# Kernel tuning notes

Hardware: AMD Instinct MI355X
Metric: run time of the kernel (lower is better)

## Reference

```python
import jax, jax.numpy as jnp
import numpy as np

B, C_IN, C_OUT, H, W = 8, 64, 64, 128, 128
G, K, PAD = 8, 3, 1
CG_OUT = C_OUT // G   # 8
CG_IN = C_IN // G     # 8


def setup_inputs() -> dict:
    key = jax.random.key(0)
    ks = jax.random.split(key, 6)
    x = jax.random.normal(ks[0], (B, C_IN, H, W), dtype=jnp.float32)
    # grouped 1x1 conv weights, stored as (groups, out_per_group, in_per_group)
    scale = (2.0 / C_OUT) ** 0.5  # kaiming fan_out
    Wq = jax.random.normal(ks[1], (G, CG_OUT, CG_IN), dtype=jnp.float32) * scale
    Wk = jax.random.normal(ks[2], (G, CG_OUT, CG_IN), dtype=jnp.float32) * scale
    Wv = jax.random.normal(ks[3], (G, CG_OUT, CG_IN), dtype=jnp.float32) * scale
    h_emb = jax.random.normal(ks[4], (G, CG_OUT // 2, 1, 1, K, 1), dtype=jnp.float32)
    w_emb = jax.random.normal(ks[5], (G, CG_OUT // 2, 1, 1, 1, K), dtype=jnp.float32)
    return {"x": x, "Wq": Wq, "Wk": Wk, "Wv": Wv, "h_emb": h_emb, "w_emb": w_emb}


def _gconv1x1(x, Wt):
    # grouped 1x1 conv: x (B,C,H,W) -> (B,G,Cg,H,W)
    b, c, h, w = x.shape
    xg = x.reshape(b, G, c // G, h, w)
    return jnp.einsum('bgihw,goi->bgohw', xg, Wt)


def _unfold(t):
    # t: (B,G,Cg,H+2p,W+2p) -> (B,G,Cg,H,W,K*K), window index = i*K + j (h-major,
    # matching torch unfold(2).unfold(3).view)
    slices = [t[..., i:i + H, j:j + W] for i in range(K) for j in range(K)]
    return jnp.stack(slices, axis=-1)


def reference(x, Wq, Wk, Wv, h_emb, w_emb):
    x_pad = jnp.pad(x, ((0, 0), (0, 0), (PAD, PAD), (PAD, PAD)))
    q = _gconv1x1(x, Wq)            # (B,G,Cg,H,W)
    kf = _gconv1x1(x_pad, Wk)       # (B,G,Cg,H+2,W+2)
    vf = _gconv1x1(x_pad, Wv)
    kp = _unfold(kf)                # (B,G,Cg,H,W,K^2)
    vp = _unfold(vf)
    # relative position embedding: h half broadcast over w, w half over h
    he = jnp.broadcast_to(h_emb, (G, CG_OUT // 2, 1, 1, K, K))
    we = jnp.broadcast_to(w_emb, (G, CG_OUT // 2, 1, 1, K, K))
    emb = jnp.concatenate([he, we], axis=1).reshape(G, CG_OUT, 1, 1, K * K)
    logits = q[..., None] * (kp + emb[None])       # (B,G,Cg,H,W,K^2)
    attn = jax.nn.softmax(logits, axis=-1)
    out = jnp.sum(attn * vp, axis=-1)              # (B,G,Cg,H,W)
    return out.reshape(x.shape[0], C_OUT, H, W)
```

## Files before the change

### kernel.cpp

```cpp
#include <hip/hip_runtime.h>


typedef float v2f __attribute__((ext_vector_type(2)));
typedef float v4f __attribute__((ext_vector_type(4)));

#define HH 128
#define WW 128
#define HW (HH * WW)
#define PT 34
#define PTS 38
#define LOG2E 1.44269504088896f

__device__ __forceinline__ float sload(float v) {
    return __uint_as_float(__builtin_amdgcn_readfirstlane(__float_as_uint(v)));
}

__device__ __forceinline__ v4f exp2v4(v4f a) {
    v4f r;
    r.x = __builtin_amdgcn_exp2f(a.x);
    r.y = __builtin_amdgcn_exp2f(a.y);
    r.z = __builtin_amdgcn_exp2f(a.z);
    r.w = __builtin_amdgcn_exp2f(a.w);
    return r;
}

__global__ __launch_bounds__(256) void sab_fused(
    const float* __restrict__ x,
    const float* __restrict__ Wq,
    const float* __restrict__ Wk,
    const float* __restrict__ Wv,
    const float* __restrict__ h_emb,
    const float* __restrict__ w_emb,
    float* __restrict__ out)
{
    __shared__ v2f kv[2][PT][PTS];

    const int bid0 = blockIdx.x;
    const int work = (bid0 & 7) * 512 + (bid0 >> 3);
    const int c0   = (work & 3) << 1;
    const int tile = (work >> 2) & 15;
    const int bg   = work >> 6;
    const int g    = bg & 7;
    const int h0   = (tile >> 2) << 5;
    const int w0   = (tile & 3) << 5;
    const int tid  = threadIdx.x;
    const int ty   = tid >> 3;
    const int x0   = (tid & 7) << 2;

    float wk[2][8], wv[2][8], wq[2][8], eb[2][9];
    #pragma unroll
    for (int cc = 0; cc < 2; cc++) {
        const int c = c0 + cc;
        #pragma unroll
        for (int i = 0; i < 8; i++) {
            wk[cc][i] = sload(Wk[g * 64 + c * 8 + i]);
            wv[cc][i] = sload(Wv[g * 64 + c * 8 + i]);
            wq[cc][i] = sload(Wq[g * 64 + c * 8 + i]);
        }
        #pragma unroll
        for (int p = 0; p < 9; p++) {
            eb[cc][p] = sload((c < 4) ? h_emb[(g * 4 + c) * 3 + p / 3]
                                      : w_emb[(g * 4 + c - 4) * 3 + p % 3]);
        }
    }

    const float* xb = x + (size_t)bg * 8 * HW;
    const int ibase = (h0 + ty) * WW + (w0 + x0);

    v4f xi[8];
    #pragma unroll
    for (int i = 0; i < 8; i++)
        xi[i] = *reinterpret_cast<const v4f*>(xb + i * HW + ibase);

    v4f kk0 = 0.f, vv0 = 0.f, qq0 = 0.f, kk1 = 0.f, vv1 = 0.f, qq1 = 0.f;
    #pragma unroll
    for (int i = 0; i < 8; i++) {
        const v4f xv = xi[i];
        kk0 += wk[0][i] * xv;  vv0 += wv[0][i] * xv;  qq0 += wq[0][i] * xv;
        kk1 += wk[1][i] * xv;  vv1 += wv[1][i] * xv;  qq1 += wq[1][i] * xv;
    }
    #pragma unroll
    for (int px = 0; px < 4; px++) {
        kv[0][ty + 1][x0 + 1 + px] = (v2f){kk0[px], vv0[px]};
        kv[1][ty + 1][x0 + 1 + px] = (v2f){kk1[px], vv1[px]};
    }
    const v4f q0 = qq0 * LOG2E;
    const v4f q1 = qq1 * LOG2E;

    if (tid < 132) {
        int hpy, hpx;
        if (tid < 34)       { hpy = 0;        hpx = tid; }
        else if (tid < 68)  { hpy = 33;       hpx = tid - 34; }
        else if (tid < 100) { hpy = tid - 67; hpx = 0; }
        else                { hpy = tid - 99; hpx = 33; }
        const int gh = h0 + hpy - 1, gw = w0 + hpx - 1;
        const bool ok = (gh >= 0) & (gh < HH) & (gw >= 0) & (gw < WW);
        const int base = gh * WW + gw;
        float hk0 = 0.f, hv0 = 0.f, hk1 = 0.f, hv1 = 0.f;
        #pragma unroll
        for (int i = 0; i < 8; i++) {
            const float xv = ok ? xb[i * HW + base] : 0.0f;
            hk0 = fmaf(wk[0][i], xv, hk0);
            hv0 = fmaf(wv[0][i], xv, hv0);
            hk1 = fmaf(wk[1][i], xv, hk1);
            hv1 = fmaf(wv[1][i], xv, hv1);
        }
        kv[0][hpy][hpx] = (v2f){hk0, hv0};
        kv[1][hpy][hpx] = (v2f){hk1, hv1};
    }
    __syncthreads();

    v4f s0 = 0.f, o0 = 0.f, s1 = 0.f, o1 = 0.f;
    #pragma unroll
    for (int dh = 0; dh < 3; dh++) {
        #pragma unroll
        for (int cc = 0; cc < 2; cc++) {
            const v2f* row = &kv[cc][ty + dh][x0];
            const v4f a = *reinterpret_cast<const v4f*>(row);
            const v4f bq = *reinterpret_cast<const v4f*>(row + 2);
            const v4f cq = *reinterpret_cast<const v4f*>(row + 4);

            const v4f kd0 = {a.x, a.z, bq.x, bq.z};
            const v4f vd0 = {a.y, a.w, bq.y, bq.w};
            const v4f kd1 = {a.z, bq.x, bq.z, cq.x};
            const v4f vd1 = {a.w, bq.y, bq.w, cq.y};
            const v4f kd2 = {bq.x, bq.z, cq.x, cq.z};
            const v4f vd2 = {bq.y, bq.w, cq.y, cq.w};

            const v4f q4 = cc ? q1 : q0;
            v4f e;
            e = exp2v4(q4 * (kd0 + eb[cc][dh * 3 + 0]));
            if (cc) { s1 += e; o1 += e * vd0; } else { s0 += e; o0 += e * vd0; }
            e = exp2v4(q4 * (kd1 + eb[cc][dh * 3 + 1]));
            if (cc) { s1 += e; o1 += e * vd1; } else { s0 += e; o0 += e * vd1; }
            e = exp2v4(q4 * (kd2 + eb[cc][dh * 3 + 2]));
            if (cc) { s1 += e; o1 += e * vd2; } else { s0 += e; o0 += e * vd2; }
        }
    }

    v4f r0, r1;
    #pragma unroll
    for (int px = 0; px < 4; px++) {
        r0[px] = o0[px] * __builtin_amdgcn_rcpf(s0[px]);
        r1[px] = o1[px] * __builtin_amdgcn_rcpf(s1[px]);
    }
    *reinterpret_cast<v4f*>(out + (size_t)(bg * 8 + c0 + 0) * HW + ibase) = r0;
    *reinterpret_cast<v4f*>(out + (size_t)(bg * 8 + c0 + 1) * HW + ibase) = r1;
}

extern "C" void kernel_launch(void* const* d_in, const int* in_sizes, int n_in,
                              void* d_out, int out_size, void* d_ws, size_t ws_size,
                              hipStream_t stream) {
    const float* x    = (const float*)d_in[0];
    const float* Wq   = (const float*)d_in[1];
    const float* Wk   = (const float*)d_in[2];
    const float* Wv   = (const float*)d_in[3];
    const float* h_e  = (const float*)d_in[4];
    const float* w_e  = (const float*)d_in[5];
    float* out = (float*)d_out;

    dim3 grid(8 * 8 * 16 * 4);
    dim3 block(256);
    sab_fused<<<grid, block, 0, stream>>>(x, Wq, Wk, Wv, h_e, w_e, out);
}
```

Measured before the change: 28.75 us.

## Loop over all output-channel pairs per block to reuse loaded input tile

Each block now handles all four channel pairs of a group for its spatial tile, looping over chunks instead of launching a separate block per pair. The 8-channel input tile and halo values are loaded once into registers and reused across the four chunks, which cuts redundant global reads of x by four. The trade-offs are a grid four times smaller (1024 blocks), extra barriers between chunks that serialise the shared-memory reuse, and more live registers.

```diff
diff --git a/kernel.cpp b/kernel.cpp
--- a/kernel.cpp
+++ b/kernel.cpp
@@ -36,10 +36,9 @@
     __shared__ v2f kv[2][PT][PTS];
 
     const int bid0 = blockIdx.x;
-    const int work = (bid0 & 7) * 512 + (bid0 >> 3);
-    const int c0   = (work & 3) << 1;
-    const int tile = (work >> 2) & 15;
-    const int bg   = work >> 6;
+    const int work = (bid0 & 7) * 128 + (bid0 >> 3);
+    const int tile = work & 15;
+    const int bg   = work >> 4;
     const int g    = bg & 7;
     const int h0   = (tile >> 2) << 5;
     const int w0   = (tile & 3) << 5;
@@ -47,105 +46,119 @@
     const int ty   = tid >> 3;
     const int x0   = (tid & 7) << 2;
 
-    float wk[2][8], wv[2][8], wq[2][8], eb[2][9];
-    #pragma unroll
-    for (int cc = 0; cc < 2; cc++) {
-        const int c = c0 + cc;
-        #pragma unroll
-        for (int i = 0; i < 8; i++) {
-            wk[cc][i] = sload(Wk[g * 64 + c * 8 + i]);
-            wv[cc][i] = sload(Wv[g * 64 + c * 8 + i]);
-            wq[cc][i] = sload(Wq[g * 64 + c * 8 + i]);
-        }
-        #pragma unroll
-        for (int p = 0; p < 9; p++) {
-            eb[cc][p] = sload((c < 4) ? h_emb[(g * 4 + c) * 3 + p / 3]
-                                      : w_emb[(g * 4 + c - 4) * 3 + p % 3]);
-        }
-    }
-
     const float* xb = x + (size_t)bg * 8 * HW;
     const int ibase = (h0 + ty) * WW + (w0 + x0);
+
+    int hpy = 0, hpx = 0;
+    const bool is_halo = tid < 132;
+    if (is_halo) {
+        if (tid < 34)       { hpy = 0;        hpx = tid; }
+        else if (tid < 68)  { hpy = 33;       hpx = tid - 34; }
+        else if (tid < 100) { hpy = tid - 67; hpx = 0; }
+        else                { hpy = tid - 99; hpx = 33; }
+    }
+    const int hgh = h0 + hpy - 1, hgw = w0 + hpx - 1;
+    const bool hok = is_halo & (hgh >= 0) & (hgh < HH) & (hgw >= 0) & (hgw < WW);
+    const int hbase = hgh * WW + hgw;
+
+    float hx[8];
+    #pragma unroll
+    for (int i = 0; i < 8; i++)
+        hx[i] = hok ? xb[i * HW + hbase] : 0.0f;
 
     v4f xi[8];
     #pragma unroll
     for (int i = 0; i < 8; i++)
         xi[i] = *reinterpret_cast<const v4f*>(xb + i * HW + ibase);
 
-    v4f kk0 = 0.f, vv0 = 0.f, qq0 = 0.f, kk1 = 0.f, vv1 = 0.f, qq1 = 0.f;
-    #pragma unroll
-    for (int i = 0; i < 8; i++) {
-        const v4f xv = xi[i];
-        kk0 += wk[0][i] * xv;  vv0 += wv[0][i] * xv;  qq0 += wq[0][i] * xv;
-        kk1 += wk[1][i] * xv;  vv1 += wv[1][i] * xv;  qq1 += wq[1][i] * xv;
-    }
-    #pragma unroll
-    for (int px = 0; px < 4; px++) {
-        kv[0][ty + 1][x0 + 1 + px] = (v2f){kk0[px], vv0[px]};
-        kv[1][ty + 1][x0 + 1 + px] = (v2f){kk1[px], vv1[px]};
-    }
-    const v4f q0 = qq0 * LOG2E;
-    const v4f q1 = qq1 * LOG2E;
+    #pragma unroll 1
+    for (int chunk = 0; chunk < 4; ++chunk) {
+        if (chunk) __syncthreads();
+        const int c0 = chunk << 1;
 
-    if (tid < 132) {
-        int hpy, hpx;
-        if (tid < 34)       { hpy = 0;        hpx = tid; }
-        else if (tid < 68)  { hpy = 33;       hpx = tid - 34; }
-        else if (tid < 100) { hpy = tid - 67; hpx = 0; }
-        else                { hpy = tid - 99; hpx = 33; }
-        const int gh = h0 + hpy - 1, gw = w0 + hpx - 1;
-        const bool ok = (gh >= 0) & (gh < HH) & (gw >= 0) & (gw < WW);
-        const int base = gh * WW + gw;
-        float hk0 = 0.f, hv0 = 0.f, hk1 = 0.f, hv1 = 0.f;
+        float wk[2][8], wv[2][8], wq[2][8], eb[2][9];
+        #pragma unroll
+        for (int cc = 0; cc < 2; cc++) {
+            const int c = c0 + cc;
+            #pragma unroll
+            for (int i = 0; i < 8; i++) {
+                wk[cc][i] = sload(Wk[g * 64 + c * 8 + i]);
+                wv[cc][i] = sload(Wv[g * 64 + c * 8 + i]);
+                wq[cc][i] = sload(Wq[g * 64 + c * 8 + i]);
+            }
+            #pragma unroll
+            for (int p = 0; p < 9; p++) {
+                eb[cc][p] = sload((c < 4) ? h_emb[(g * 4 + c) * 3 + p / 3]
+                                          : w_emb[(g * 4 + c - 4) * 3 + p % 3]);
+            }
+        }
+
+        v4f kk0 = 0.f, vv0 = 0.f, qq0 = 0.f, kk1 = 0.f, vv1 = 0.f, qq1 = 0.f;
         #pragma unroll
         for (int i = 0; i < 8; i++) {
-            const float xv = ok ? xb[i * HW + base] : 0.0f;
-            hk0 = fmaf(wk[0][i], xv, hk0);
-            hv0 = fmaf(wv[0][i], xv, hv0);
-            hk1 = fmaf(wk[1][i], xv, hk1);
-            hv1 = fmaf(wv[1][i], xv, hv1);
+            const v4f xv = xi[i];
+            kk0 += wk[0][i] * xv;  vv0 += wv[0][i] * xv;  qq0 += wq[0][i] * xv;
+            kk1 += wk[1][i] * xv;  vv1 += wv[1][i] * xv;  qq1 += wq[1][i] * xv;
         }
-        kv[0][hpy][hpx] = (v2f){hk0, hv0};
-        kv[1][hpy][hpx] = (v2f){hk1, hv1};
+        #pragma unroll
+        for (int px = 0; px < 4; px++) {
+            kv[0][ty + 1][x0 + 1 + px] = (v2f){kk0[px], vv0[px]};
+            kv[1][ty + 1][x0 + 1 + px] = (v2f){kk1[px], vv1[px]};
+        }
+        const v4f q0 = qq0 * LOG2E;
+        const v4f q1 = qq1 * LOG2E;
+
+        if (is_halo) {
+            float hk0 = 0.f, hv0 = 0.f, hk1 = 0.f, hv1 = 0.f;
+            #pragma unroll
+            for (int i = 0; i < 8; i++) {
+                hk0 = fmaf(wk[0][i], hx[i], hk0);
+                hv0 = fmaf(wv[0][i], hx[i], hv0);
+                hk1 = fmaf(wk[1][i], hx[i], hk1);
+                hv1 = fmaf(wv[1][i], hx[i], hv1);
+            }
+            kv[0][hpy][hpx] = (v2f){hk0, hv0};
+            kv[1][hpy][hpx] = (v2f){hk1, hv1};
+        }
+        __syncthreads();
+
+        v4f s0 = 0.f, o0 = 0.f, s1 = 0.f, o1 = 0.f;
+        #pragma unroll
+        for (int dh = 0; dh < 3; dh++) {
+            #pragma unroll
+            for (int cc = 0; cc < 2; cc++) {
+                const v2f* row = &kv[cc][ty + dh][x0];
+                const v4f a  = *reinterpret_cast<const v4f*>(row);
+                const v4f bq = *reinterpret_cast<const v4f*>(row + 2);
+                const v4f cq = *reinterpret_cast<const v4f*>(row + 4);
+
+                const v4f kd0 = {a.x, a.z, bq.x, bq.z};
+                const v4f vd0 = {a.y, a.w, bq.y, bq.w};
+                const v4f kd1 = {a.z, bq.x, bq.z, cq.x};
+                const v4f vd1 = {a.w, bq.y, bq.w, cq.y};
+                const v4f kd2 = {bq.x, bq.z, cq.x, cq.z};
+                const v4f vd2 = {bq.y, bq.w, cq.y, cq.w};
+
+                const v4f q4 = cc ? q1 : q0;
+                v4f e;
+                e = exp2v4(q4 * (kd0 + eb[cc][dh * 3 + 0]));
+                if (cc) { s1 += e; o1 += e * vd0; } else { s0 += e; o0 += e * vd0; }
+                e = exp2v4(q4 * (kd1 + eb[cc][dh * 3 + 1]));
+                if (cc) { s1 += e; o1 += e * vd1; } else { s0 += e; o0 += e * vd1; }
+                e = exp2v4(q4 * (kd2 + eb[cc][dh * 3 + 2]));
+                if (cc) { s1 += e; o1 += e * vd2; } else { s0 += e; o0 += e * vd2; }
+            }
+        }
+
+        v4f r0, r1;
+        #pragma unroll
+        for (int px = 0; px < 4; px++) {
+            r0[px] = o0[px] * __builtin_amdgcn_rcpf(s0[px]);
+            r1[px] = o1[px] * __builtin_amdgcn_rcpf(s1[px]);
+        }
+        *reinterpret_cast<v4f*>(out + (size_t)(bg * 8 + c0 + 0) * HW + ibase) = r0;
+        *reinterpret_cast<v4f*>(out + (size_t)(bg * 8 + c0 + 1) * HW + ibase) = r1;
     }
-    __syncthreads();
-
-    v4f s0 = 0.f, o0 = 0.f, s1 = 0.f, o1 = 0.f;
-    #pragma unroll
-    for (int dh = 0; dh < 3; dh++) {
-        #pragma unroll
-        for (int cc = 0; cc < 2; cc++) {
-            const v2f* row = &kv[cc][ty + dh][x0];
-            const v4f a = *reinterpret_cast<const v4f*>(row);
-            const v4f bq = *reinterpret_cast<const v4f*>(row + 2);
-            const v4f cq = *reinterpret_cast<const v4f*>(row + 4);
-
-            const v4f kd0 = {a.x, a.z, bq.x, bq.z};
-            const v4f vd0 = {a.y, a.w, bq.y, bq.w};
-            const v4f kd1 = {a.z, bq.x, bq.z, cq.x};
-            const v4f vd1 = {a.w, bq.y, bq.w, cq.y};
-            const v4f kd2 = {bq.x, bq.z, cq.x, cq.z};
-            const v4f vd2 = {bq.y, bq.w, cq.y, cq.w};
-
-            const v4f q4 = cc ? q1 : q0;
-            v4f e;
-            e = exp2v4(q4 * (kd0 + eb[cc][dh * 3 + 0]));
-            if (cc) { s1 += e; o1 += e * vd0; } else { s0 += e; o0 += e * vd0; }
-            e = exp2v4(q4 * (kd1 + eb[cc][dh * 3 + 1]));
-            if (cc) { s1 += e; o1 += e * vd1; } else { s0 += e; o0 += e * vd1; }
-            e = exp2v4(q4 * (kd2 + eb[cc][dh * 3 + 2]));
-            if (cc) { s1 += e; o1 += e * vd2; } else { s0 += e; o0 += e * vd2; }
-        }
-    }
-
-    v4f r0, r1;
-    #pragma unroll
-    for (int px = 0; px < 4; px++) {
-        r0[px] = o0[px] * __builtin_amdgcn_rcpf(s0[px]);
-        r1[px] = o1[px] * __builtin_amdgcn_rcpf(s1[px]);
-    }
-    *reinterpret_cast<v4f*>(out + (size_t)(bg * 8 + c0 + 0) * HW + ibase) = r0;
-    *reinterpret_cast<v4f*>(out + (size_t)(bg * 8 + c0 + 1) * HW + ibase) = r1;
 }
 
 extern "C" void kernel_launch(void* const* d_in, const int* in_sizes, int n_in,
@@ -159,7 +172,7 @@
     const float* w_e  = (const float*)d_in[5];
     float* out = (float*)d_out;
 
-    dim3 grid(8 * 8 * 16 * 4);
+    dim3 grid(8 * 8 * 16);
     dim3 block(256);
     sab_fused<<<grid, block, 0, stream>>>(x, Wq, Wk, Wv, h_e, w_e, out);
 }
```

New measurement: 31.11 us. 1.08x slower.
